# Kernel optimization log

Hardware: AMD Instinct MI355X
Metric: run time of the kernel (lower is better)

The kernel has to match this reference:

```python
import jax, jax.numpy as jnp
import numpy as np

B, N, D, E, H = 8, 128, 64, 3, 256
L = E + 1  # edge label 0 = 'no edge' (dropped by edge_types[:, 1:])
DEC_OUT = 64


def setup_inputs() -> dict:
    key = jax.random.key(0)
    ks = jax.random.split(key, 8)
    node_states = jax.random.normal(ks[0], (B, 1, N, D), dtype=jnp.float32)
    # one-hot edge-type labels [B, N, N, L]
    type_ids = jax.random.randint(ks[1], (B, N, N), 0, L)
    edges = jax.nn.one_hot(type_ids, L, dtype=jnp.float32)
    def lin(k, fan_in, shape):
        return jax.random.normal(k, shape, dtype=jnp.float32) / jnp.sqrt(jnp.float32(fan_in))
    return {
        "node_states": node_states,
        "edges": edges,
        # per-edge-type encoder MLP (2 layers, relu after each)
        "We1": lin(ks[2], 2 * D, (E, 2 * D, H)),
        "be1": jnp.zeros((E, H), dtype=jnp.float32),
        "We2": lin(ks[3], H, (E, H, H)),
        "be2": jnp.zeros((E, H), dtype=jnp.float32),
        # node decoder MLP (2 layers, relu after each)
        "Wd1": lin(ks[4], D + H, (D + H, H)),
        "bd1": jnp.zeros((H,), dtype=jnp.float32),
        "Wd2": lin(ks[5], H, (H, DEC_OUT)),
        "bd2": jnp.zeros((DEC_OUT,), dtype=jnp.float32),
    }


def reference(node_states, edges, We1, be1, We2, be2, Wd1, bd1, Wd2, bd2):
    b, _, n, d = node_states.shape
    ns = node_states[:, 0]  # [B, N, D]
    # NodePropagator: for fully-connected edges, the one-hot matmuls are a
    # gather: edge e = (i, j) gets [ns[i], ns[j]] (flat index i*N + j).
    msg_src = jnp.broadcast_to(ns[:, :, None, :], (b, n, n, d))  # source i
    msg_tgt = jnp.broadcast_to(ns[:, None, :, :], (b, n, n, d))  # target j
    node_msgs = jnp.concatenate([msg_src, msg_tgt], -1).reshape(b, n * n, 2 * d)
    # EdgeEncoder: one 2-layer relu MLP per edge type -> [B, E, N^2, H]
    h = jax.nn.relu(jnp.einsum("bmd,edh->bemh", node_msgs, We1) + be1[None, :, None, :])
    h = jax.nn.relu(jnp.einsum("bemh,ehk->bemk", h, We2) + be2[None, :, None, :])
    # mask by edge-type indicator; type 0 (no edge) is dropped
    edge_types = jnp.transpose(edges.reshape(b, n * n, L), (0, 2, 1))  # [B, L, N^2]
    edge_msgs = h * edge_types[:, 1:, :, None]  # [B, E, N^2, H]
    # EdgeAggregator: edge_targets^T matmul = scatter-sum over sources i per
    # target j, then sum over edge types (dim 1, keepdim).
    aggr = edge_msgs.reshape(b, E, n, n, H).sum(axis=2)  # [B, E, N, H]
    aggr = aggr.sum(axis=1, keepdims=True)  # [B, 1, N, H]
    # node decoder
    dec_in = jnp.concatenate([node_states, aggr], -1)  # [B, 1, N, D+H]
    out = jax.nn.relu(dec_in @ Wd1 + bd1)
    out = jax.nn.relu(out @ Wd2 + bd2)
    return out  # [B, 1, N, DEC_OUT]
```

## Files before the change

kernel.cpp:

```cpp
#include <hip/hip_runtime.h>

#define NB 8
#define NN 128
#define ND 64
#define NE 3
#define NH 256
#define NOUT 64

typedef short bf16x8_t __attribute__((ext_vector_type(8)));
typedef float f32x4_t __attribute__((ext_vector_type(4)));
typedef unsigned short ushort_t;

static __device__ __forceinline__ unsigned short f2bf(float f) {
    unsigned u = __float_as_uint(f);
    u += 0x7FFFu + ((u >> 16) & 1u);
    return (unsigned short)(u >> 16);
}
static __device__ __forceinline__ unsigned pk2bf(float a, float b) {
    return (unsigned)f2bf(a) | ((unsigned)f2bf(b) << 16);
}
static __device__ __forceinline__ float bflo(unsigned u) { return __uint_as_float(u << 16); }
static __device__ __forceinline__ float bfhi(unsigned u) { return __uint_as_float(u & 0xffff0000u); }

static __device__ __forceinline__ bf16x8_t a_genp(uint4 pv, float4 q0, float4 q1) {
    union { uint4 u; bf16x8_t v; } r;
    r.u.x = pk2bf(fmaxf(bflo(pv.x) + q0.x, 0.f), fmaxf(bfhi(pv.x) + q0.y, 0.f));
    r.u.y = pk2bf(fmaxf(bflo(pv.y) + q0.z, 0.f), fmaxf(bfhi(pv.y) + q0.w, 0.f));
    r.u.z = pk2bf(fmaxf(bflo(pv.z) + q1.x, 0.f), fmaxf(bfhi(pv.z) + q1.y, 0.f));
    r.u.w = pk2bf(fmaxf(bflo(pv.w) + q1.z, 0.f), fmaxf(bfhi(pv.w) + q1.w, 0.f));
    return r.v;
}

#define IT 16
__global__ __launch_bounds__(256) void prep_kernel(
    const float* __restrict__ We2, const float* __restrict__ ns,
    const float* __restrict__ We1, const float* __restrict__ be1,
    const float* __restrict__ edges,
    ushort_t* __restrict__ We2p,
    ushort_t* __restrict__ P, float* __restrict__ Q,
    ushort_t* __restrict__ list_ws, int4* __restrict__ cnts_ws)
{
    const int t = threadIdx.x;
    const int blk = blockIdx.x;

    if (blk < 48) {
        __shared__ float slab[256][16];
        const int e = blk >> 4, nfg = blk & 15;
        const int n0 = nfg * 16;
#pragma unroll
        for (int it = 0; it < 16; it++) {
            const int k = (t >> 4) + it * 16;
            slab[k][t & 15] = We2[((size_t)e * NH + k) * NH + n0 + (t & 15)];
        }
        __syncthreads();
        ushort_t* dst = We2p + ((size_t)e * 16 + nfg) * 4096;
#pragma unroll
        for (int it = 0; it < 16; it++) {
            const int idx = it * 256 + t;
            const int kk = idx >> 9;
            const int ln = (idx >> 3) & 63;
            const int jj = idx & 7;
            const int k = kk * 32 + (ln >> 4) * 8 + jj;
            dst[idx] = f2bf(slab[k][ln & 15]);
        }
        return;
    }
    if (blk < 240) {
        __shared__ float ns_lds[IT][ND];
        const int blk2 = blk - 48;
        const int itile = blk2 & 7;
        const int e = (blk2 >> 3) % NE;
        const int b = blk2 / 24;
        const int i0 = itile * IT;
        for (int x = t; x < IT * ND; x += 256)
            ns_lds[x / ND][x % ND] = ns[(size_t)(b * NN + i0 + x / ND) * ND + (x % ND)];
        __syncthreads();
        const int h = t;
        float accP[IT], accQ[IT];
        const float bias = be1[e * NH + h];
#pragma unroll
        for (int m = 0; m < IT; m++) { accP[m] = 0.f; accQ[m] = bias; }
        const float* W1 = We1 + (size_t)e * 2 * ND * NH + h;
        for (int d = 0; d < ND; d++) {
            const float w1 = W1[(size_t)d * NH];
            const float w2 = W1[(size_t)(ND + d) * NH];
#pragma unroll
            for (int m = 0; m < IT; m++) {
                accP[m] = fmaf(ns_lds[m][d], w1, accP[m]);
                accQ[m] = fmaf(ns_lds[m][d], w2, accQ[m]);
            }
        }
#pragma unroll
        for (int m = 0; m < IT; m++) {
            const size_t idx = ((size_t)((b * NE + e) * NN) + i0 + m) * NH + h;
            P[idx] = f2bf(accP[m]);
            Q[idx] = accQ[m];
        }
        return;
    }
    {
        __shared__ unsigned long long wm[2][NE];
        const int pb = blk - 240;
        const int b = pb >> 7, j = pb & 127;
        const int lane = t & 63, wave = t >> 6;
        int ecls = -1;
        if (t < 128) {
            const float4 ev = *(const float4*)(edges + ((size_t)(b * NN + t) * NN + j) * 4);
            ecls = ev.y > 0.5f ? 0 : (ev.z > 0.5f ? 1 : (ev.w > 0.5f ? 2 : -1));
#pragma unroll
            for (int ee = 0; ee < NE; ee++) {
                unsigned long long m = __ballot(ecls == ee);
                if (lane == 0) wm[wave][ee] = m;
            }
        }
        __syncthreads();
        const int c0 = __popcll(wm[0][0]) + __popcll(wm[1][0]);
        const int c1 = __popcll(wm[0][1]) + __popcll(wm[1][1]);
        const int c2 = __popcll(wm[0][2]) + __popcll(wm[1][2]);
        if (t < 128 && ecls >= 0) {
            const unsigned long long lower = (1ull << lane) - 1ull;
            int pos = __popcll(wm[wave][ecls] & lower);
            if (wave == 1) pos += __popcll(wm[0][ecls]);
            pos += (ecls > 0 ? c0 : 0) + (ecls > 1 ? c1 : 0);
            list_ws[(size_t)pb * NN + pos] = (ushort_t)t;
        }
        if (t == 0) { int4 cc; cc.x = c0; cc.y = c1; cc.z = c2; cc.w = 0; cnts_ws[pb] = cc; }
    }
}

__global__ __launch_bounds__(1024) void gemm_kernel(
    const ushort_t* __restrict__ Pbf,
    const float* __restrict__ Qf,
    const ushort_t* __restrict__ We2p,
    const float* __restrict__ be2,
    const ushort_t* __restrict__ list_ws,
    const int4* __restrict__ cnts_ws,
    float* __restrict__ aggrP)
{
    const int blk = blockIdx.x;
    const int nh = blk & 1;
    const int jq = (blk >> 1) & 15;
    const int b  = blk >> 5;
    const int tid = threadIdx.x;
    const int lane = tid & 63;
    const int wave = tid >> 6;
    const int j  = jq * 8 + (wave >> 1);
    const int rh = wave & 1;

    __shared__ __align__(16) char Lds[139264];
    ushort_t* Bp = (ushort_t*)(Lds + 65536);
    float* Ql = (float*)(Lds + 131072);

    for (int e = 0; e < NE; e++) {
        __syncthreads();
        {
            const ushort_t* Ps = Pbf + (size_t)(b * NE + e) * NN * NH;
#pragma unroll
            for (int it = 0; it < 4; it++) {
                const int c = it * 1024 + tid;
                const int row = c >> 5, c16 = c & 31;
                const uint4 v = *(const uint4*)(Ps + c * 8);
                *(uint4*)(Lds + row * 512 + ((c16 * 16) ^ ((row & 7) << 4))) = v;
            }
            const ushort_t* Bs = We2p + ((size_t)e * 16 + nh * 8) * 4096;
#pragma unroll
            for (int it = 0; it < 4; it++) {
                const int o = (it * 1024 + tid) * 8;
                *(uint4*)&Bp[o] = *(const uint4*)&Bs[o];
            }
            if (tid < 512) {
                const float* Qs = Qf + (size_t)((b * NE + e) * NN + jq * 8) * NH + tid * 4;
                *(float4*)(Ql + tid * 4) = *(const float4*)Qs;
            }
        }
        __syncthreads();

        const int4 cc = cnts_ws[b * NN + j];
        const int ce = e == 0 ? cc.x : (e == 1 ? cc.y : cc.z);
        const int start = (e > 0 ? cc.x : 0) + (e > 1 ? cc.y : 0);
        const ushort_t* Lj = list_ws + (size_t)(b * NN + j) * NN + start;
        const float* Qj = Ql + (wave >> 1) * NH;

        float bb[8];
#pragma unroll
        for (int nf = 0; nf < 8; nf++)
            bb[nf] = be2[e * NH + nh * 128 + nf * 16 + (lane & 15)];

        float rsum[8];
#pragma unroll
        for (int nf = 0; nf < 8; nf++) rsum[nf] = 0.f;

        if (ce > 0) {
            const int F = (ce + 15) >> 4;
            for (int f = rh; f < F; f += 2) {
                int p = f * 16 + (lane & 15);
                p = p < ce ? p : ce - 1;
                const int row = Lj[p];
                const int rbase = row * 512;
                const int sw = (row & 7) << 4;

                f32x4_t acc[8];
                const f32x4_t z4 = {0.f, 0.f, 0.f, 0.f};
#pragma unroll
                for (int nf = 0; nf < 8; nf++) acc[nf] = z4;

#pragma unroll 2
                for (int kk = 0; kk < 8; kk++) {
                    const int grp = (lane >> 4) * 16;
                    const uint4 pv = *(const uint4*)(Lds + rbase + ((kk * 64 + grp) ^ sw));
                    const int qo = kk * 32 + (lane >> 4) * 8;
                    const float4 q0 = *(const float4*)(Qj + qo);
                    const float4 q1 = *(const float4*)(Qj + qo + 4);
                    const bf16x8_t af = a_genp(pv, q0, q1);
#pragma unroll
                    for (int nf = 0; nf < 8; nf++) {
                        const bf16x8_t bfr = *(const bf16x8_t*)(&Bp[(nf * 8 + kk) * 512 + lane * 8]);
                        acc[nf] = __builtin_amdgcn_mfma_f32_16x16x32_bf16(af, bfr, acc[nf], 0, 0, 0);
                    }
                }
#pragma unroll
                for (int nf = 0; nf < 8; nf++) {
                    float s = 0.f;
#pragma unroll
                    for (int r = 0; r < 4; r++) {
                        const int pos = f * 16 + ((lane >> 4) << 2) + r;
                        if (pos < ce) s += fmaxf(acc[nf][r] + bb[nf], 0.f);
                    }
                    s += __shfl_xor(s, 16, 64);
                    s += __shfl_xor(s, 32, 64);
                    if (lane < 16) rsum[nf] += s;
                }
            }
        }
        if (lane < 16) {
            float* dst = aggrP + ((size_t)((b * NE + e) * NN + j) * 2 + rh) * NH + nh * 128 + lane;
#pragma unroll
            for (int nf = 0; nf < 8; nf++) dst[nf * 16] = rsum[nf];
        }
    }
}

__global__ __launch_bounds__(256) void dec_kernel(
    const float* __restrict__ ns,
    const float* __restrict__ aggrP,
    const float* __restrict__ Wd1, const float* __restrict__ bd1,
    const float* __restrict__ Wd2, const float* __restrict__ bd2,
    float* __restrict__ out)
{
    const int b = blockIdx.x >> 5;
    const int jq = blockIdx.x & 31;
    const int tid = threadIdx.x;
    __shared__ __align__(16) float xs[4][320];
    __shared__ __align__(16) float o1s[4][NH];

    for (int x = tid; x < 4 * 320; x += 256) {
        const int jj = x / 320, k = x % 320;
        const int j = jq * 4 + jj;
        float v;
        if (k < ND) v = ns[(size_t)(b * NN + j) * ND + k];
        else {
            const int c = k - ND;
            v = 0.f;
#pragma unroll
            for (int e = 0; e < NE; e++) {
                const size_t base = ((size_t)((b * NE + e) * NN + j) * 2) * NH + c;
                v += aggrP[base] + aggrP[base + NH];
            }
        }
        xs[jj][k] = v;
    }
    __syncthreads();
    {
        const int n = tid;
        float acc[4];
        const float b1 = bd1[n];
#pragma unroll
        for (int jj = 0; jj < 4; jj++) acc[jj] = b1;
        for (int k4 = 0; k4 < 80; k4++) {
            const float w0 = Wd1[(size_t)(k4 * 4 + 0) * NH + n];
            const float w1 = Wd1[(size_t)(k4 * 4 + 1) * NH + n];
            const float w2 = Wd1[(size_t)(k4 * 4 + 2) * NH + n];
            const float w3 = Wd1[(size_t)(k4 * 4 + 3) * NH + n];
#pragma unroll
            for (int jj = 0; jj < 4; jj++) {
                const float4 xv = *(const float4*)(&xs[jj][k4 * 4]);
                acc[jj] = fmaf(xv.x, w0, fmaf(xv.y, w1, fmaf(xv.z, w2, fmaf(xv.w, w3, acc[jj]))));
            }
        }
#pragma unroll
        for (int jj = 0; jj < 4; jj++) o1s[jj][n] = fmaxf(acc[jj], 0.f);
    }
    __syncthreads();
    {
        const int jj = tid >> 6, col = tid & 63;
        float a = bd2[col];
        for (int h4 = 0; h4 < 64; h4++) {
            const float4 ov = *(const float4*)(&o1s[jj][h4 * 4]);
            a = fmaf(ov.x, Wd2[(size_t)(h4 * 4 + 0) * NOUT + col], a);
            a = fmaf(ov.y, Wd2[(size_t)(h4 * 4 + 1) * NOUT + col], a);
            a = fmaf(ov.z, Wd2[(size_t)(h4 * 4 + 2) * NOUT + col], a);
            a = fmaf(ov.w, Wd2[(size_t)(h4 * 4 + 3) * NOUT + col], a);
        }
        const int j = jq * 4 + jj;
        out[(size_t)(b * NN + j) * NOUT + col] = fmaxf(a, 0.f);
    }
}

extern "C" void kernel_launch(void* const* d_in, const int* in_sizes, int n_in,
                              void* d_out, int out_size, void* d_ws, size_t ws_size,
                              hipStream_t stream)
{
    const float* ns    = (const float*)d_in[0];
    const float* edges = (const float*)d_in[1];
    const float* We1   = (const float*)d_in[2];
    const float* be1   = (const float*)d_in[3];
    const float* We2   = (const float*)d_in[4];
    const float* be2   = (const float*)d_in[5];
    const float* Wd1   = (const float*)d_in[6];
    const float* bd1   = (const float*)d_in[7];
    const float* Wd2   = (const float*)d_in[8];
    const float* bd2   = (const float*)d_in[9];
    float* outp = (float*)d_out;

    ushort_t* Pbf = (ushort_t*)d_ws;
    float* Qf = (float*)(Pbf + (size_t)NB * NE * NN * NH);
    ushort_t* We2p = (ushort_t*)(Qf + (size_t)NB * NE * NN * NH);
    ushort_t* list_ws = We2p + (size_t)NE * NH * NH;
    int4* cnts_ws = (int4*)(list_ws + (size_t)NB * NN * NN);
    float* aggrP = (float*)(cnts_ws + NB * NN);

    hipLaunchKernelGGL(prep_kernel, dim3(1264), dim3(256), 0, stream,
                       We2, ns, We1, be1, edges, We2p, Pbf, Qf, list_ws, cnts_ws);
    hipLaunchKernelGGL(gemm_kernel, dim3(256), dim3(1024), 0, stream,
                       Pbf, Qf, We2p, be2, list_ws, cnts_ws, aggrP);
    hipLaunchKernelGGL(dec_kernel, dim3(256), dim3(256), 0, stream,
                       ns, aggrP, Wd1, bd1, Wd2, bd2, outp);
}
```

Before: 81.95 us.

## Switch edge GEMM to 32x32x16 MFMA with bf16 Q and per-wave N split

The edge-encoder second-layer GEMM moves from 16x16x32 MFMA tiles to 32x32x16 tiles. Each wave now handles 32 source rows and 64 output columns instead of splitting rows across two waves, and the We2 prepack layout changes to match. Q is stored as bf16 instead of fp32, which halves its global and LDS traffic, and the partial aggregates are written once per (e,j) so the decoder no longer sums two halves. The cost is extra rounding on Q and coarser 32-row tiles, which waste more work when the per-type edge counts are not multiples of 32.

```diff
diff --git a/kernel.cpp b/kernel.cpp
--- a/kernel.cpp
+++ b/kernel.cpp
@@ -8,7 +8,7 @@
 #define NOUT 64
 
 typedef short bf16x8_t __attribute__((ext_vector_type(8)));
-typedef float f32x4_t __attribute__((ext_vector_type(4)));
+typedef float f32x16_t __attribute__((ext_vector_type(16)));
 typedef unsigned short ushort_t;
 
 static __device__ __forceinline__ unsigned short f2bf(float f) {
@@ -22,12 +22,12 @@
 static __device__ __forceinline__ float bflo(unsigned u) { return __uint_as_float(u << 16); }
 static __device__ __forceinline__ float bfhi(unsigned u) { return __uint_as_float(u & 0xffff0000u); }
 
-static __device__ __forceinline__ bf16x8_t a_genp(uint4 pv, float4 q0, float4 q1) {
+static __device__ __forceinline__ bf16x8_t a_gen(uint4 pv, uint4 qv) {
     union { uint4 u; bf16x8_t v; } r;
-    r.u.x = pk2bf(fmaxf(bflo(pv.x) + q0.x, 0.f), fmaxf(bfhi(pv.x) + q0.y, 0.f));
-    r.u.y = pk2bf(fmaxf(bflo(pv.y) + q0.z, 0.f), fmaxf(bfhi(pv.y) + q0.w, 0.f));
-    r.u.z = pk2bf(fmaxf(bflo(pv.z) + q1.x, 0.f), fmaxf(bfhi(pv.z) + q1.y, 0.f));
-    r.u.w = pk2bf(fmaxf(bflo(pv.w) + q1.z, 0.f), fmaxf(bfhi(pv.w) + q1.w, 0.f));
+    r.u.x = pk2bf(fmaxf(bflo(pv.x) + bflo(qv.x), 0.f), fmaxf(bfhi(pv.x) + bfhi(qv.x), 0.f));
+    r.u.y = pk2bf(fmaxf(bflo(pv.y) + bflo(qv.y), 0.f), fmaxf(bfhi(pv.y) + bfhi(qv.y), 0.f));
+    r.u.z = pk2bf(fmaxf(bflo(pv.z) + bflo(qv.z), 0.f), fmaxf(bfhi(pv.z) + bfhi(qv.z), 0.f));
+    r.u.w = pk2bf(fmaxf(bflo(pv.w) + bflo(qv.w), 0.f), fmaxf(bfhi(pv.w) + bfhi(qv.w), 0.f));
     return r.v;
 }
 
@@ -37,37 +37,38 @@
     const float* __restrict__ We1, const float* __restrict__ be1,
     const float* __restrict__ edges,
     ushort_t* __restrict__ We2p,
-    ushort_t* __restrict__ P, float* __restrict__ Q,
+    ushort_t* __restrict__ P, ushort_t* __restrict__ Q,
     ushort_t* __restrict__ list_ws, int4* __restrict__ cnts_ws)
 {
     const int t = threadIdx.x;
     const int blk = blockIdx.x;
 
-    if (blk < 48) {
-        __shared__ float slab[256][16];
-        const int e = blk >> 4, nfg = blk & 15;
-        const int n0 = nfg * 16;
-#pragma unroll
-        for (int it = 0; it < 16; it++) {
-            const int k = (t >> 4) + it * 16;
-            slab[k][t & 15] = We2[((size_t)e * NH + k) * NH + n0 + (t & 15)];
-        }
-        __syncthreads();
-        ushort_t* dst = We2p + ((size_t)e * 16 + nfg) * 4096;
-#pragma unroll
-        for (int it = 0; it < 16; it++) {
+    if (blk < 24) {
+        __shared__ float slab[256][33];
+        const int e = blk >> 3, ntg = blk & 7;
+        const int n0 = ntg * 32;
+#pragma unroll
+        for (int it = 0; it < 32; it++) {
+            const int idx = it * 256 + t;
+            const int k = idx >> 5, col = idx & 31;
+            slab[k][col] = We2[((size_t)e * NH + k) * NH + n0 + col];
+        }
+        __syncthreads();
+        ushort_t* dst = We2p + ((size_t)e * 8 + ntg) * 8192;
+#pragma unroll
+        for (int it = 0; it < 32; it++) {
             const int idx = it * 256 + t;
             const int kk = idx >> 9;
-            const int ln = (idx >> 3) & 63;
-            const int jj = idx & 7;
-            const int k = kk * 32 + (ln >> 4) * 8 + jj;
-            dst[idx] = f2bf(slab[k][ln & 15]);
+            const int rem = idx & 511;
+            const int ln = rem >> 3, x = rem & 7;
+            const int k = kk * 16 + (ln >> 5) * 8 + x;
+            dst[idx] = f2bf(slab[k][ln & 31]);
         }
         return;
     }
-    if (blk < 240) {
+    if (blk < 216) {
         __shared__ float ns_lds[IT][ND];
-        const int blk2 = blk - 48;
+        const int blk2 = blk - 24;
         const int itile = blk2 & 7;
         const int e = (blk2 >> 3) % NE;
         const int b = blk2 / 24;
@@ -94,13 +95,13 @@
         for (int m = 0; m < IT; m++) {
             const size_t idx = ((size_t)((b * NE + e) * NN) + i0 + m) * NH + h;
             P[idx] = f2bf(accP[m]);
-            Q[idx] = accQ[m];
+            Q[idx] = f2bf(accQ[m]);
         }
         return;
     }
     {
         __shared__ unsigned long long wm[2][NE];
-        const int pb = blk - 240;
+        const int pb = blk - 216;
         const int b = pb >> 7, j = pb & 127;
         const int lane = t & 63, wave = t >> 6;
         int ecls = -1;
@@ -130,12 +131,12 @@
 
 __global__ __launch_bounds__(1024) void gemm_kernel(
     const ushort_t* __restrict__ Pbf,
-    const float* __restrict__ Qf,
+    const ushort_t* __restrict__ Qbf,
     const ushort_t* __restrict__ We2p,
     const float* __restrict__ be2,
     const ushort_t* __restrict__ list_ws,
     const int4* __restrict__ cnts_ws,
-    float* __restrict__ aggrP)
+    float* __restrict__ aggr3)
 {
     const int blk = blockIdx.x;
     const int nh = blk & 1;
@@ -145,11 +146,13 @@
     const int lane = tid & 63;
     const int wave = tid >> 6;
     const int j  = jq * 8 + (wave >> 1);
-    const int rh = wave & 1;
-
-    __shared__ __align__(16) char Lds[139264];
+    const int qd = wave & 1;
+    const int hi = lane >> 5;
+    const int l31 = lane & 31;
+
+    __shared__ __align__(16) char Lds[135168];
     ushort_t* Bp = (ushort_t*)(Lds + 65536);
-    float* Ql = (float*)(Lds + 131072);
+    ushort_t* Ql = (ushort_t*)(Lds + 131072);
 
     for (int e = 0; e < NE; e++) {
         __syncthreads();
@@ -162,15 +165,15 @@
                 const uint4 v = *(const uint4*)(Ps + c * 8);
                 *(uint4*)(Lds + row * 512 + ((c16 * 16) ^ ((row & 7) << 4))) = v;
             }
-            const ushort_t* Bs = We2p + ((size_t)e * 16 + nh * 8) * 4096;
+            const ushort_t* Bs = We2p + ((size_t)e * 8 + nh * 4) * 8192;
 #pragma unroll
             for (int it = 0; it < 4; it++) {
                 const int o = (it * 1024 + tid) * 8;
                 *(uint4*)&Bp[o] = *(const uint4*)&Bs[o];
             }
-            if (tid < 512) {
-                const float* Qs = Qf + (size_t)((b * NE + e) * NN + jq * 8) * NH + tid * 4;
-                *(float4*)(Ql + tid * 4) = *(const float4*)Qs;
+            if (tid < 256) {
+                const ushort_t* Qs = Qbf + (size_t)((b * NE + e) * NN + jq * 8) * NH + tid * 8;
+                *(uint4*)(Ql + tid * 8) = *(const uint4*)Qs;
             }
         }
         __syncthreads();
@@ -179,70 +182,65 @@
         const int ce = e == 0 ? cc.x : (e == 1 ? cc.y : cc.z);
         const int start = (e > 0 ? cc.x : 0) + (e > 1 ? cc.y : 0);
         const ushort_t* Lj = list_ws + (size_t)(b * NN + j) * NN + start;
-        const float* Qj = Ql + (wave >> 1) * NH;
-
-        float bb[8];
-#pragma unroll
-        for (int nf = 0; nf < 8; nf++)
-            bb[nf] = be2[e * NH + nh * 128 + nf * 16 + (lane & 15)];
-
-        float rsum[8];
-#pragma unroll
-        for (int nf = 0; nf < 8; nf++) rsum[nf] = 0.f;
+        const ushort_t* Qj = Ql + (wave >> 1) * NH;
+
+        float bb[2];
+#pragma unroll
+        for (int nt = 0; nt < 2; nt++)
+            bb[nt] = be2[e * NH + nh * 128 + qd * 64 + nt * 32 + l31];
+
+        float rsum[2] = {0.f, 0.f};
 
         if (ce > 0) {
-            const int F = (ce + 15) >> 4;
-            for (int f = rh; f < F; f += 2) {
-                int p = f * 16 + (lane & 15);
+            const int T = (ce + 31) >> 5;
+            for (int tt = 0; tt < T; tt++) {
+                int p = tt * 32 + l31;
                 p = p < ce ? p : ce - 1;
                 const int row = Lj[p];
                 const int rbase = row * 512;
                 const int sw = (row & 7) << 4;
 
-                f32x4_t acc[8];
-                const f32x4_t z4 = {0.f, 0.f, 0.f, 0.f};
-#pragma unroll
-                for (int nf = 0; nf < 8; nf++) acc[nf] = z4;
+                f32x16_t acc[2];
+                const f32x16_t z16 = {0.f, 0.f, 0.f, 0.f, 0.f, 0.f, 0.f, 0.f,
+                                      0.f, 0.f, 0.f, 0.f, 0.f, 0.f, 0.f, 0.f};
+                acc[0] = z16; acc[1] = z16;
 
 #pragma unroll 2
-                for (int kk = 0; kk < 8; kk++) {
-                    const int grp = (lane >> 4) * 16;
-                    const uint4 pv = *(const uint4*)(Lds + rbase + ((kk * 64 + grp) ^ sw));
-                    const int qo = kk * 32 + (lane >> 4) * 8;
-                    const float4 q0 = *(const float4*)(Qj + qo);
-                    const float4 q1 = *(const float4*)(Qj + qo + 4);
-                    const bf16x8_t af = a_genp(pv, q0, q1);
-#pragma unroll
-                    for (int nf = 0; nf < 8; nf++) {
-                        const bf16x8_t bfr = *(const bf16x8_t*)(&Bp[(nf * 8 + kk) * 512 + lane * 8]);
-                        acc[nf] = __builtin_amdgcn_mfma_f32_16x16x32_bf16(af, bfr, acc[nf], 0, 0, 0);
+                for (int kk = 0; kk < 16; kk++) {
+                    const int xo = kk * 32 + hi * 16;
+                    const uint4 pv = *(const uint4*)(Lds + rbase + (xo ^ sw));
+                    const uint4 qv = *(const uint4*)((const char*)Qj + xo);
+                    const bf16x8_t af = a_gen(pv, qv);
+#pragma unroll
+                    for (int nt = 0; nt < 2; nt++) {
+                        const bf16x8_t bfr = *(const bf16x8_t*)(&Bp[((qd * 2 + nt) * 16 + kk) * 512 + lane * 8]);
+                        acc[nt] = __builtin_amdgcn_mfma_f32_32x32x16_bf16(af, bfr, acc[nt], 0, 0, 0);
                     }
                 }
 #pragma unroll
-                for (int nf = 0; nf < 8; nf++) {
+                for (int nt = 0; nt < 2; nt++) {
                     float s = 0.f;
 #pragma unroll
-                    for (int r = 0; r < 4; r++) {
-                        const int pos = f * 16 + ((lane >> 4) << 2) + r;
-                        if (pos < ce) s += fmaxf(acc[nf][r] + bb[nf], 0.f);
+                    for (int r = 0; r < 16; r++) {
+                        const int pos = tt * 32 + (r & 3) + 8 * (r >> 2) + 4 * hi;
+                        if (pos < ce) s += fmaxf(acc[nt][r] + bb[nt], 0.f);
                     }
-                    s += __shfl_xor(s, 16, 64);
                     s += __shfl_xor(s, 32, 64);
-                    if (lane < 16) rsum[nf] += s;
+                    rsum[nt] += s;
                 }
             }
         }
-        if (lane < 16) {
-            float* dst = aggrP + ((size_t)((b * NE + e) * NN + j) * 2 + rh) * NH + nh * 128 + lane;
-#pragma unroll
-            for (int nf = 0; nf < 8; nf++) dst[nf * 16] = rsum[nf];
+        if (lane < 32) {
+            float* dst = aggr3 + (size_t)((b * NE + e) * NN + j) * NH + nh * 128 + qd * 64 + l31;
+            dst[0] = rsum[0];
+            dst[32] = rsum[1];
         }
     }
 }
 
 __global__ __launch_bounds__(256) void dec_kernel(
     const float* __restrict__ ns,
-    const float* __restrict__ aggrP,
+    const float* __restrict__ aggr3,
     const float* __restrict__ Wd1, const float* __restrict__ bd1,
     const float* __restrict__ Wd2, const float* __restrict__ bd2,
     float* __restrict__ out)
@@ -260,12 +258,9 @@
         if (k < ND) v = ns[(size_t)(b * NN + j) * ND + k];
         else {
             const int c = k - ND;
-            v = 0.f;
-#pragma unroll
-            for (int e = 0; e < NE; e++) {
-                const size_t base = ((size_t)((b * NE + e) * NN + j) * 2) * NH + c;
-                v += aggrP[base] + aggrP[base + NH];
-            }
+            v = aggr3[(size_t)((b * NE + 0) * NN + j) * NH + c]
+              + aggr3[(size_t)((b * NE + 1) * NN + j) * NH + c]
+              + aggr3[(size_t)((b * NE + 2) * NN + j) * NH + c];
         }
         xs[jj][k] = v;
     }
@@ -323,16 +318,16 @@
     float* outp = (float*)d_out;
 
     ushort_t* Pbf = (ushort_t*)d_ws;
-    float* Qf = (float*)(Pbf + (size_t)NB * NE * NN * NH);
-    ushort_t* We2p = (ushort_t*)(Qf + (size_t)NB * NE * NN * NH);
+    ushort_t* Qbf = Pbf + (size_t)NB * NE * NN * NH;
+    ushort_t* We2p = Qbf + (size_t)NB * NE * NN * NH;
     ushort_t* list_ws = We2p + (size_t)NE * NH * NH;
     int4* cnts_ws = (int4*)(list_ws + (size_t)NB * NN * NN);
-    float* aggrP = (float*)(cnts_ws + NB * NN);
-
-    hipLaunchKernelGGL(prep_kernel, dim3(1264), dim3(256), 0, stream,
-                       We2, ns, We1, be1, edges, We2p, Pbf, Qf, list_ws, cnts_ws);
+    float* aggr3 = (float*)(cnts_ws + NB * NN);
+
+    hipLaunchKernelGGL(prep_kernel, dim3(1240), dim3(256), 0, stream,
+                       We2, ns, We1, be1, edges, We2p, Pbf, Qbf, list_ws, cnts_ws);
     hipLaunchKernelGGL(gemm_kernel, dim3(256), dim3(1024), 0, stream,
-                       Pbf, Qf, We2p, be2, list_ws, cnts_ws, aggrP);
+                       Pbf, Qbf, We2p, be2, list_ws, cnts_ws, aggr3);
     hipLaunchKernelGGL(dec_kernel, dim3(256), dim3(256), 0, stream,
-                       ns, aggrP, Wd1, bd1, Wd2, bd2, outp);
-}
+                       ns, aggr3, Wd1, bd1, Wd2, bd2, outp);
+}
```

After: 93.01 us. 13.5% more time.
